# Kernel tuning notes

Hardware: AMD Instinct MI355X
Metric: run time of the kernel (lower is better)

## Reference

```python
import jax, jax.numpy as jnp
import numpy as np

V, B, H, NH = 3, 8192, 2048, 16
HD = H // NH
EPS = 1e-5


def setup_inputs() -> dict:
    key = jax.random.key(0)
    ks = jax.random.split(key, 20)
    s = 0.02
    d = {
        "views": jax.random.normal(ks[0], (V, B, H), jnp.float32),
        # per-view query/key/value projections (torch Linear: y = x @ W.T + b)
        "Wq": jax.random.normal(ks[1], (V, H, H)) * s, "bq": jnp.zeros((V, H)),
        "Wk": jax.random.normal(ks[2], (V, H, H)) * s, "bk": jnp.zeros((V, H)),
        "Wv": jax.random.normal(ks[3], (V, H, H)) * s, "bv": jnp.zeros((V, H)),
        # per-view MultiheadAttention internal in_proj (split into q/k/v) and out_proj
        "Wiq": jax.random.normal(ks[4], (V, H, H)) * s, "biq": jnp.zeros((V, H)),
        "Wik": jax.random.normal(ks[5], (V, H, H)) * s, "bik": jnp.zeros((V, H)),
        "Wiv": jax.random.normal(ks[6], (V, H, H)) * s, "biv": jnp.zeros((V, H)),
        "Wo": jax.random.normal(ks[7], (V, H, H)) * s, "bo": jnp.zeros((V, H)),
        # fusion output linear over concatenated views
        "Wout": jax.random.normal(ks[8], (H, V * H)) * s, "bout": jnp.zeros((H,)),
        # LayerNorm
        "gamma": jnp.ones((H,)), "beta": jnp.zeros((H,)),
    }
    return d


def reference(views, Wq, bq, Wk, bk, Wv, bv, Wiq, biq, Wik, bik, Wiv, biv,
              Wo, bo, Wout, bout, gamma, beta):
    # views: [V, B, H]
    # per-view q/k/v projections applied to each view's own embedding
    q = jnp.einsum('vbh,vgh->vbg', views, Wq) + bq[:, None]      # [V,B,H]
    k_all = jnp.einsum('vbh,vgh->vbg', views, Wk) + bk[:, None]  # [V,B,H]
    v_all = jnp.einsum('vbh,vgh->vbg', views, Wv) + bv[:, None]  # [V,B,H]

    # for query view i, keys/values come from all other views (static gather)
    others = jnp.asarray(np.array([[j for j in range(V) if j != i] for i in range(V)]))
    K = k_all[others]   # [V, V-1, B, H]
    Vv = v_all[others]  # [V, V-1, B, H]

    # MultiheadAttention internal in-projections (per query-view i)
    q2 = jnp.einsum('vbh,vgh->vbg', q, Wiq) + biq[:, None]                # [V,B,H]
    k2 = jnp.einsum('vjbh,vgh->vjbg', K, Wik) + bik[:, None, None]        # [V,V-1,B,H]
    v2 = jnp.einsum('vjbh,vgh->vjbg', Vv, Wiv) + biv[:, None, None]       # [V,V-1,B,H]

    qh = q2.reshape(V, B, NH, HD)           # q_len = 1 (squeezed)
    kh = k2.reshape(V, V - 1, B, NH, HD)
    vh = v2.reshape(V, V - 1, B, NH, HD)

    scores = jnp.einsum('vbnd,vjbnd->vbnj', qh, kh) / jnp.sqrt(jnp.float32(HD))
    attn = jax.nn.softmax(scores, axis=-1)  # over the V-1 key views
    ctx = jnp.einsum('vbnj,vjbnd->vbnd', attn, vh).reshape(V, B, H)
    att_out = jnp.einsum('vbh,vgh->vbg', ctx, Wo) + bo[:, None]           # [V,B,H]

    # concat attended outputs per-sample: [B, V*H]
    fused = att_out.transpose(1, 0, 2).reshape(B, V * H)
    projected = fused @ Wout.T + bout

    # residual with first view + LayerNorm (dropout inactive / eval)
    x = views[0] + projected
    mu = jnp.mean(x, axis=-1, keepdims=True)
    var = jnp.mean(jnp.square(x - mu), axis=-1, keepdims=True)
    out = (x - mu) * jax.lax.rsqrt(var + EPS) * gamma + beta
    return out
```

## Files before the change

kernel.cpp:

```cpp
#include <hip/hip_runtime.h>
#include <hip/hip_bf16.h>

typedef __attribute__((ext_vector_type(8))) __bf16 bf16x8;
typedef __attribute__((ext_vector_type(4))) float f32x4;
typedef __hip_bfloat16 bf16_t;

#define BB 8192L
#define HH 2048L
#define BH (8192L*2048L)
#define WUNIT (2048L*2048L)
#define WT (3L*2048L*2048L)
#define LDS_TOTAL 131072

struct SlabMap { int a[6]; int w[6]; };
struct Ptrs4 { const float* in[4]; bf16_t* out[4]; };
struct FoldJob { const float* W2; const float* b1; const float* badd; float* out; int ld; };
struct FoldPack { FoldJob j[16]; };

__device__ __forceinline__ void gload_lds16(const void* g, void* l) {
    __builtin_amdgcn_global_load_lds((__attribute__((address_space(1))) void*)g,
                                     (__attribute__((address_space(3))) void*)l, 16, 0, 0);
}

template<bool OUT_F32, bool FUSEK>
__global__ __launch_bounds__(512, 1)
void gemm256(const bf16_t* __restrict__ A, int lda, long aslab, SlabMap map, int mshift,
             const bf16_t* __restrict__ Bw, int ldb,
             const float* __restrict__ bias,
             void* __restrict__ Cout, int ldc, long cslab, int K)
{
    extern __shared__ char lds[];
    const int tid  = threadIdx.x;
    const int lane = tid & 63;
    const int w    = tid >> 6;
    const int wm   = w >> 2, wn = w & 3;

    const int nwg = (int)gridDim.x;
    const int wid = (int)blockIdx.x;
    const int swz = (wid & 7) * (nwg >> 3) + (wid >> 3);
    const int bx  = swz & 7;
    const int by  = swz >> 3;

    const int  sl    = by >> mshift;
    const long rowA0 = (long)(by & ((1 << mshift) - 1)) * 256;
    const long rowB0 = (long)bx * 256;
    const bf16_t* Ab = FUSEK ? A : (A + (long)map.a[sl] * aslab);
    const bf16_t* Wb = Bw + (long)map.w[sl] * WUNIT;
    const float*  be = bias ? (bias + (long)map.w[sl] * HH) : nullptr;

    const int srow    = tid >> 3;
    const int schunk8 = ((tid & 7) ^ (srow & 7)) * 8;
    const int wuni    = w * 1024;
    const int NK = K >> 6;

    auto stageA = [&](int s) {
        char* dst = lds + (s & 1) * 65536;
        const int k0 = s << 6;
        const bf16_t* Aeff; int ka;
        if constexpr (FUSEK) { Aeff = A + (long)(k0 >> 11) * aslab; ka = k0 & 2047; }
        else                 { Aeff = Ab; ka = k0; }
        #pragma unroll
        for (int i = 0; i < 4; ++i)
            gload_lds16(Aeff + (rowA0 + i*64 + srow) * (long)lda + (ka + schunk8), dst + i*8192 + wuni);
    };
    auto stageB = [&](int s, int q) {
        char* dst = lds + (s & 1) * 65536 + 32768 + q*16384;
        const int k0 = s << 6;
        #pragma unroll
        for (int j = 0; j < 2; ++j)
            gload_lds16(Wb + (rowB0 + q*128 + j*64 + srow) * (long)ldb + (k0 + schunk8), dst + j*8192 + wuni);
    };

    f32x4 acc[8][4];
    const f32x4 zero = {0.f, 0.f, 0.f, 0.f};
    #pragma unroll
    for (int i = 0; i < 8; ++i)
        #pragma unroll
        for (int j = 0; j < 4; ++j) acc[i][j] = zero;

    stageB(0,0); stageB(0,1);
    stageA(0);
    stageB(1,0); stageB(1,1);
    asm volatile("s_waitcnt vmcnt(4)" ::: "memory");
    asm volatile("s_barrier" ::: "memory");

    const int arow16 = wm*128 + (lane & 15);
    const int brow16 = wn*64  + (lane & 15);
    const int kb     = (lane >> 4) * 16;

    #define LDSA(row, kh) (*(const bf16x8*)(bufA + (row)*128 + (((kh)*64 + kb) ^ (((row) & 7) << 4))))
    #define LDSB(row, kh) (*(const bf16x8*)(bufB + (row)*128 + (((kh)*64 + kb) ^ (((row) & 7) << 4))))

    for (int s = 0; s < NK; ++s) {
        char* bufA = lds + (s & 1) * 65536;
        char* bufB = bufA + 32768;
        bf16x8 a[4][2], b0[2][2], b1[2][2];

        if (s + 1 < NK) stageA(s + 1);
        #pragma unroll
        for (int cf = 0; cf < 2; ++cf) {
            const int r = brow16 + cf*16;
            #pragma unroll
            for (int kh = 0; kh < 2; ++kh) b0[cf][kh] = LDSB(r, kh);
        }
        #pragma unroll
        for (int rf = 0; rf < 4; ++rf) {
            const int r = arow16 + rf*16;
            #pragma unroll
            for (int kh = 0; kh < 2; ++kh) a[rf][kh] = LDSA(r, kh);
        }
        asm volatile("s_barrier" ::: "memory");
        __builtin_amdgcn_sched_barrier(0);
        __builtin_amdgcn_s_setprio(1);
        #pragma unroll
        for (int kh = 0; kh < 2; ++kh)
            #pragma unroll
            for (int rf = 0; rf < 4; ++rf)
                #pragma unroll
                for (int cf = 0; cf < 2; ++cf)
                    acc[rf][cf] = __builtin_amdgcn_mfma_f32_16x16x32_bf16(a[rf][kh], b0[cf][kh], acc[rf][cf], 0, 0, 0);
        __builtin_amdgcn_s_setprio(0);

        #pragma unroll
        for (int cf = 0; cf < 2; ++cf) {
            const int r = brow16 + 32 + cf*16;
            #pragma unroll
            for (int kh = 0; kh < 2; ++kh) b1[cf][kh] = LDSB(r, kh);
        }
        asm volatile("s_barrier" ::: "memory");
        __builtin_amdgcn_sched_barrier(0);
        __builtin_amdgcn_s_setprio(1);
        #pragma unroll
        for (int kh = 0; kh < 2; ++kh)
            #pragma unroll
            for (int rf = 0; rf < 4; ++rf)
                #pragma unroll
                for (int cf = 0; cf < 2; ++cf)
                    acc[rf][2+cf] = __builtin_amdgcn_mfma_f32_16x16x32_bf16(a[rf][kh], b1[cf][kh], acc[rf][2+cf], 0, 0, 0);
        __builtin_amdgcn_s_setprio(0);

        if (s + 2 < NK) stageB(s + 2, 0);
        #pragma unroll
        for (int rf = 0; rf < 4; ++rf) {
            const int r = arow16 + 64 + rf*16;
            #pragma unroll
            for (int kh = 0; kh < 2; ++kh) a[rf][kh] = LDSA(r, kh);
        }
        asm volatile("s_barrier" ::: "memory");
        __builtin_amdgcn_sched_barrier(0);
        __builtin_amdgcn_s_setprio(1);
        #pragma unroll
        for (int kh = 0; kh < 2; ++kh)
            #pragma unroll
            for (int rf = 0; rf < 4; ++rf)
                #pragma unroll
                for (int cf = 0; cf < 2; ++cf)
                    acc[4+rf][cf] = __builtin_amdgcn_mfma_f32_16x16x32_bf16(a[rf][kh], b0[cf][kh], acc[4+rf][cf], 0, 0, 0);
        __builtin_amdgcn_s_setprio(0);

        if (s + 2 < NK) stageB(s + 2, 1);
        if (s + 1 < NK) {
            if (s + 2 < NK) asm volatile("s_waitcnt vmcnt(4)" ::: "memory");
            else            asm volatile("s_waitcnt vmcnt(0)" ::: "memory");
            asm volatile("s_barrier" ::: "memory");
            __builtin_amdgcn_sched_barrier(0);
        }
        __builtin_amdgcn_s_setprio(1);
        #pragma unroll
        for (int kh = 0; kh < 2; ++kh)
            #pragma unroll
            for (int rf = 0; rf < 4; ++rf)
                #pragma unroll
                for (int cf = 0; cf < 2; ++cf)
                    acc[4+rf][2+cf] = __builtin_amdgcn_mfma_f32_16x16x32_bf16(a[rf][kh], b1[cf][kh], acc[4+rf][2+cf], 0, 0, 0);
        __builtin_amdgcn_s_setprio(0);
    }
    #undef LDSA
    #undef LDSB

    const long crow0 = rowA0 + wm*128 + ((lane >> 4) * 4);
    const int  ccol0 = (int)rowB0 + wn*64 + (lane & 15);
    const long cbase = (long)sl * cslab;
    #pragma unroll
    for (int rf = 0; rf < 8; ++rf) {
        #pragma unroll
        for (int cf = 0; cf < 4; ++cf) {
            const int col = ccol0 + cf*16;
            const float bv = be ? be[col] : 0.f;
            #pragma unroll
            for (int r = 0; r < 4; ++r) {
                const long row = crow0 + rf*16 + r;
                const float val = acc[rf][cf][r] + bv;
                if constexpr (OUT_F32) ((float*)Cout)[cbase + row*(long)ldc + col] = val;
                else ((bf16_t*)Cout)[cbase + row*(long)ldc + col] = __float2bfloat16(val);
            }
        }
    }
}

__global__ __launch_bounds__(256)
void f2b_kernel(const float* __restrict__ in, bf16_t* __restrict__ out, long n)
{
    long i = ((long)blockIdx.x * 256 + threadIdx.x) * 4;
    const long stride = (long)gridDim.x * 256 * 4;
    for (; i < n; i += stride) {
        const float4 v = *(const float4*)(in + i);
        __hip_bfloat162 lo, hi;
        lo.x = __float2bfloat16(v.x); lo.y = __float2bfloat16(v.y);
        hi.x = __float2bfloat16(v.z); hi.y = __float2bfloat16(v.w);
        *(__hip_bfloat162*)(out + i)     = lo;
        *(__hip_bfloat162*)(out + i + 2) = hi;
    }
}

__global__ __launch_bounds__(256)
void f2b4_kernel(Ptrs4 p)
{
    const long total = 4 * WT;
    long i = ((long)blockIdx.x * 256 + threadIdx.x) * 4;
    const long stride = (long)gridDim.x * 256 * 4;
    for (; i < total; i += stride) {
        const int  t   = (int)(i / WT);
        const long off = i - (long)t * WT;
        const float4 v = *(const float4*)(p.in[t] + off);
        __hip_bfloat162 lo, hi;
        lo.x = __float2bfloat16(v.x); lo.y = __float2bfloat16(v.y);
        hi.x = __float2bfloat16(v.z); hi.y = __float2bfloat16(v.w);
        *(__hip_bfloat162*)(p.out[t] + off)     = lo;
        *(__hip_bfloat162*)(p.out[t] + off + 2) = hi;
    }
}

__global__ __launch_bounds__(256)
void f2bT4_kernel(Ptrs4 p)
{
    __shared__ float sm[64][65];
    const int gmat = blockIdx.x >> 10;
    const int t    = gmat / 3, m = gmat % 3;
    const int tile = blockIdx.x & 1023;
    const int tr   = tile >> 5, tc = tile & 31;
    const int lr = threadIdx.x >> 4;
    const int lc = (threadIdx.x & 15) * 4;
    const float* src = p.in[t] + (long)m*WUNIT + ((long)tr*64)*2048 + tc*64;
    #pragma unroll
    for (int it = 0; it < 4; ++it) {
        const int r = lr + it*16;
        const float4 v = *(const float4*)(src + (long)r*2048 + lc);
        sm[r][lc] = v.x; sm[r][lc+1] = v.y; sm[r][lc+2] = v.z; sm[r][lc+3] = v.w;
    }
    __syncthreads();
    bf16_t* dst = p.out[t] + (long)m*WUNIT + ((long)tc*64)*2048 + tr*64;
    #pragma unroll
    for (int it = 0; it < 4; ++it) {
        const int r = lr + it*16;
        __hip_bfloat162 p0, p1;
        p0.x = __float2bfloat16(sm[lc+0][r]); p0.y = __float2bfloat16(sm[lc+1][r]);
        p1.x = __float2bfloat16(sm[lc+2][r]); p1.y = __float2bfloat16(sm[lc+3][r]);
        *(__hip_bfloat162*)(dst + (long)r*2048 + lc)     = p0;
        *(__hip_bfloat162*)(dst + (long)r*2048 + lc + 2) = p1;
    }
}

__global__ __launch_bounds__(256)
void biasfold_all(FoldPack p)
{
    const FoldJob jb = p.j[blockIdx.x >> 11];
    const int g2 = blockIdx.x & 2047;
    const int t  = threadIdx.x;
    float s = 0.f;
    for (int k = t; k < jb.ld; k += 256) s += jb.W2[(long)g2*jb.ld + k] * jb.b1[k];
    #pragma unroll
    for (int off = 32; off > 0; off >>= 1) s += __shfl_xor(s, off);
    __shared__ float rs[4];
    if ((t & 63) == 0) rs[t >> 6] = s;
    __syncthreads();
    if (t == 0) jb.out[g2] = rs[0] + rs[1] + rs[2] + rs[3] + jb.badd[g2];
}

__global__ __launch_bounds__(256)
void attn_kernel(const bf16_t* __restrict__ q2, const bf16_t* __restrict__ k2,
                 const bf16_t* __restrict__ v2, bf16_t* __restrict__ ctx, int bshift)
{
    const long gw = (long)blockIdx.x * 4 + (threadIdx.x >> 6);
    const int lane = threadIdx.x & 63;
    const int  v_  = (int)(gw >> (bshift + 4));
    const long rem = gw & ((1L << (bshift + 4)) - 1);
    const long b   = rem >> 4;
    const int  n   = (int)(rem & 15);
    const long base = ((((long)v_ << bshift) + b)) * HH + (long)n * 128 + lane * 2;

    const __hip_bfloat162 qv = *(const __hip_bfloat162*)(q2 + base);
    const float q0 = __bfloat162float(qv.x), q1 = __bfloat162float(qv.y);
    float s[2], va[2], vb[2];
    #pragma unroll
    for (int j = 0; j < 2; ++j) {
        const long kb = ((((long)(v_*2 + j) << bshift) + b)) * HH + (long)n * 128 + lane * 2;
        const __hip_bfloat162 kv = *(const __hip_bfloat162*)(k2 + kb);
        float p = q0 * __bfloat162float(kv.x) + q1 * __bfloat162float(kv.y);
        #pragma unroll
        for (int off = 32; off > 0; off >>= 1) p += __shfl_xor(p, off);
        s[j] = p;
        const __hip_bfloat162 vv = *(const __hip_bfloat162*)(v2 + kb);
        va[j] = __bfloat162float(vv.x); vb[j] = __bfloat162float(vv.y);
    }
    const float scale = 0.08838834764831845f;
    const float s0 = s[0] * scale, s1 = s[1] * scale;
    const float m  = fmaxf(s0, s1);
    const float e0 = expf(s0 - m), e1 = expf(s1 - m);
    const float inv = 1.0f / (e0 + e1);
    const float a0 = e0 * inv, a1 = e1 * inv;
    __hip_bfloat162 o;
    o.x = __float2bfloat16(a0 * va[0] + a1 * va[1]);
    o.y = __float2bfloat16(a0 * vb[0] + a1 * vb[1]);
    *(__hip_bfloat162*)(ctx + base) = o;
}

__global__ __launch_bounds__(256)
void ln_kernel(const float* __restrict__ proj, const float* __restrict__ v0,
               const float* __restrict__ gamma, const float* __restrict__ beta,
               float* __restrict__ out)
{
    const long b = blockIdx.x;
    const int t = threadIdx.x;
    const float* pr = proj + b * HH;
    const float* vw = v0 + b * HH;
    float x[8]; float s = 0.f, s2 = 0.f;
    #pragma unroll
    for (int k = 0; k < 8; ++k) {
        const int idx = t + k * 256;
        x[k] = vw[idx] + pr[idx];
        s += x[k]; s2 += x[k] * x[k];
    }
    #pragma unroll
    for (int off = 32; off > 0; off >>= 1) { s += __shfl_xor(s, off); s2 += __shfl_xor(s2, off); }
    __shared__ float rs[4], rs2[4];
    if ((t & 63) == 0) { rs[t >> 6] = s; rs2[t >> 6] = s2; }
    __syncthreads();
    s  = rs[0] + rs[1] + rs[2] + rs[3];
    s2 = rs2[0] + rs2[1] + rs2[2] + rs2[3];
    const float mu  = s * (1.0f / 2048.0f);
    const float var = s2 * (1.0f / 2048.0f) - mu * mu;
    const float rstd = rsqrtf(var + 1e-5f);
    #pragma unroll
    for (int k = 0; k < 8; ++k) {
        const int idx = t + k * 256;
        out[b * HH + idx] = (x[k] - mu) * rstd * gamma[idx] + beta[idx];
    }
}

extern "C" void kernel_launch(void* const* d_in, const int* in_sizes, int n_in,
                              void* d_out, int out_size, void* d_ws, size_t ws_size,
                              hipStream_t stream)
{
    const float* views = (const float*)d_in[0];
    const float* Wq   = (const float*)d_in[1];  const float* bq   = (const float*)d_in[2];
    const float* Wk   = (const float*)d_in[3];  const float* bk   = (const float*)d_in[4];
    const float* Wv   = (const float*)d_in[5];  const float* bv   = (const float*)d_in[6];
    const float* Wiq  = (const float*)d_in[7];  const float* biq  = (const float*)d_in[8];
    const float* Wik  = (const float*)d_in[9];  const float* bik  = (const float*)d_in[10];
    const float* Wiv  = (const float*)d_in[11]; const float* biv  = (const float*)d_in[12];
    const float* Wo   = (const float*)d_in[13]; const float* bo   = (const float*)d_in[14];
    const float* Wout = (const float*)d_in[15]; const float* bout = (const float*)d_in[16];
    const float* gamma= (const float*)d_in[17]; const float* beta = (const float*)d_in[18];

    static bool attr_set = false;
    if (!attr_set) {
        hipFuncSetAttribute((const void*)gemm256<false,false>,
                            hipFuncAttributeMaxDynamicSharedMemorySize, LDS_TOTAL);
        hipFuncSetAttribute((const void*)gemm256<true,true>,
                            hipFuncAttributeMaxDynamicSharedMemorySize, LDS_TOTAL);
        attr_set = true;
    }

    char* ws = (char*)d_ws;
    bf16_t* WQ2  = (bf16_t*)ws;
    bf16_t* WK2  = WQ2 + 3*WUNIT;
    bf16_t* WV2  = WK2 + 6*WUNIT;
    bf16_t* WFIN = WV2 + 6*WUNIT;
    float*  BQ2  = (float*)(WFIN + 3*WUNIT);
    float*  BK2  = BQ2 + 3*HH;
    float*  BV2  = BK2 + 6*HH;
    float*  BFIN = BV2 + 6*HH;
    const long FIXED = 18L*WUNIT*2 + 16L*HH*4;

    char* R = ws + FIXED;
    bf16_t* WIQ   = (bf16_t*)R;
    bf16_t* WIK   = WIQ  + 3*WUNIT;
    bf16_t* WIV   = WIK  + 3*WUNIT;
    bf16_t* WOUTB = WIV  + 3*WUNIT;
    bf16_t* WQT   = WOUTB+ 3*WUNIT;
    bf16_t* WKT   = WQT  + 3*WUNIT;
    bf16_t* WVT   = WKT  + 3*WUNIT;
    bf16_t* WOT   = WVT  + 3*WUNIT;

    const long scratch = 24L*WUNIT*2;
    long Bc = 8192;
    while (Bc > 256) {
        long need = Bc * 73728L; if (need < scratch) need = scratch;
        if (FIXED + need <= (long)ws_size) break;
        Bc >>= 1;
    }
    const int mshift = __builtin_ctzl((unsigned long)Bc) - 8;
    const int bshift = __builtin_ctzl((unsigned long)Bc);
    const long S1 = Bc * HH;

    bf16_t* VBF = (bf16_t*)R;
    bf16_t* Q2B = VBF + 3*S1;
    bf16_t* K2  = Q2B + 3*S1;
    bf16_t* V2  = K2  + 6*S1;
    float*  PROJ= (float*)K2;

    const SlabMap mp3  = {{0,1,2,0,0,0},{0,1,2,0,0,0}};
    const SlabMap mp6k = {{1,2,0,2,0,1},{0,1,2,3,4,5}};
    const SlabMap mpfk = {{0,0,1,1,2,2},{1,2,0,2,0,1}};
    const SlabMap mp1  = {{0,0,0,0,0,0},{0,0,0,0,0,0}};
    const int oth[3][2] = {{1,2},{0,2},{0,1}};

    {
        Ptrs4 c1 = {{Wiq, Wik, Wiv, Wout}, {WIQ, WIK, WIV, WOUTB}};
        f2b4_kernel<<<8192, 256, 0, stream>>>(c1);
        Ptrs4 c2 = {{Wq, Wk, Wv, Wo}, {WQT, WKT, WVT, WOT}};
        f2bT4_kernel<<<12288, 256, 0, stream>>>(c2);
    }
    gemm256<false,false><<<192, 512, LDS_TOTAL, stream>>>(WIQ, 2048, WUNIT, mp3,  3, WQT, 2048, nullptr, (void*)WQ2, 2048, WUNIT, 2048);
    gemm256<false,false><<<384, 512, LDS_TOTAL, stream>>>(WIK, 2048, WUNIT, mpfk, 3, WKT, 2048, nullptr, (void*)WK2, 2048, WUNIT, 2048);
    gemm256<false,false><<<384, 512, LDS_TOTAL, stream>>>(WIV, 2048, WUNIT, mpfk, 3, WVT, 2048, nullptr, (void*)WV2, 2048, WUNIT, 2048);
    gemm256<false,false><<<192, 512, LDS_TOTAL, stream>>>(WOUTB, 6144, 2048, mp3, 3, WOT, 2048, nullptr, (void*)WFIN, 6144, 2048, 2048);

    {
        FoldPack fp;
        for (int v = 0; v < 3; ++v)
            fp.j[v] = { Wiq + (long)v*WUNIT, bq + v*HH, biq + v*HH, BQ2 + v*HH, 2048 };
        for (int v = 0; v < 3; ++v)
            for (int j = 0; j < 2; ++j) {
                const int p = v*2 + j, o = oth[v][j];
                fp.j[3 + p] = { Wik + (long)v*WUNIT, bk + o*HH, bik + v*HH, BK2 + p*HH, 2048 };
                fp.j[9 + p] = { Wiv + (long)v*WUNIT, bv + o*HH, biv + v*HH, BV2 + p*HH, 2048 };
            }
        fp.j[15] = { Wout, bo, bout, BFIN, 6144 };
        biasfold_all<<<32768, 256, 0, stream>>>(fp);
    }

    const int nwg3 = 8 * 3 * (int)(Bc >> 8);
    const int nwg6 = 8 * 6 * (int)(Bc >> 8);
    const int nwg1 = 8 * 1 * (int)(Bc >> 8);
    const int vgrid = (int)((S1 / 1024 > 8192) ? 8192 : S1 / 1024);

    for (long b0 = 0; b0 < BB; b0 += Bc) {
        if (Bc == 8192) {
            f2b_kernel<<<8192, 256, 0, stream>>>(views, VBF, 3*BH);
        } else {
            for (int v = 0; v < 3; ++v)
                f2b_kernel<<<vgrid, 256, 0, stream>>>(views + v*BH + b0*HH, VBF + v*S1, S1);
        }
        gemm256<false,false><<<nwg3, 512, LDS_TOTAL, stream>>>(VBF, 2048, S1, mp3,  mshift, WQ2, 2048, BQ2, (void*)Q2B, 2048, S1, 2048);
        gemm256<false,false><<<nwg6, 512, LDS_TOTAL, stream>>>(VBF, 2048, S1, mp6k, mshift, WK2, 2048, BK2, (void*)K2,  2048, S1, 2048);
        gemm256<false,false><<<nwg6, 512, LDS_TOTAL, stream>>>(VBF, 2048, S1, mp6k, mshift, WV2, 2048, BV2, (void*)V2,  2048, S1, 2048);
        attn_kernel<<<(int)(12*Bc), 256, 0, stream>>>(Q2B, K2, V2, VBF, bshift);
        gemm256<true,true><<<nwg1, 512, LDS_TOTAL, stream>>>(VBF, 2048, S1, mp1, mshift, WFIN, 6144, BFIN, (void*)PROJ, 2048, 0, 6144);
        ln_kernel<<<(int)Bc, 256, 0, stream>>>(PROJ, views + b0*HH, gamma, beta, ((float*)d_out) + b0*HH);
    }
}
```

Measured before the change: 1.699 ms.

## Triple-buffer A tiles in GEMM and merge weight-fold GEMMs into one launch

Result: faster. 1.647 ms (-3.1%).

```diff
diff --git a/kernel.cpp b/kernel.cpp
--- a/kernel.cpp
+++ b/kernel.cpp
@@ -10,16 +10,179 @@
 #define BH (8192L*2048L)
 #define WUNIT (2048L*2048L)
 #define WT (3L*2048L*2048L)
-#define LDS_TOTAL 131072
+#define LDS_TOTAL 163840
 
 struct SlabMap { int a[6]; int w[6]; };
 struct Ptrs4 { const float* in[4]; bf16_t* out[4]; };
 struct FoldJob { const float* W2; const float* b1; const float* badd; float* out; int ld; };
 struct FoldPack { FoldJob j[16]; };
+struct GJob { const bf16_t* A; const bf16_t* Bw; bf16_t* C; int lda; int ldc; };
+struct GJobs { GJob j[18]; };
 
 __device__ __forceinline__ void gload_lds16(const void* g, void* l) {
     __builtin_amdgcn_global_load_lds((__attribute__((address_space(1))) void*)g,
                                      (__attribute__((address_space(3))) void*)l, 16, 0, 0);
+}
+
+template<bool OUT_F32, bool FUSEK>
+__device__ __forceinline__ void gemm_core(
+    const bf16_t* __restrict__ A, int lda, long aslab,
+    const bf16_t* __restrict__ Wb, int ldb,
+    const float* __restrict__ be,
+    void* __restrict__ Cout, int ldc,
+    long rowA0, long rowB0, int K, char* lds)
+{
+    const int tid  = threadIdx.x;
+    const int lane = tid & 63;
+    const int w    = tid >> 6;
+    const int wm   = w >> 2, wn = w & 3;
+
+    const int srow    = tid >> 3;
+    const int schunk8 = ((tid & 7) ^ (srow & 7)) * 8;
+    const int wuni    = w * 1024;
+    const int NK = K >> 6;
+
+    auto stageA = [&](int s) {
+        char* dst = lds + (s % 3) * 32768;
+        const int k0 = s << 6;
+        const bf16_t* Aeff; int ka;
+        if constexpr (FUSEK) { Aeff = A + (long)(k0 >> 11) * aslab; ka = k0 & 2047; }
+        else                 { Aeff = A; ka = k0; }
+        #pragma unroll
+        for (int i = 0; i < 4; ++i)
+            gload_lds16(Aeff + (rowA0 + i*64 + srow) * (long)lda + (ka + schunk8), dst + i*8192 + wuni);
+    };
+    auto stageB = [&](int s, int q) {
+        char* dst = lds + 98304 + (s & 1) * 32768 + q*16384;
+        const int k0 = s << 6;
+        #pragma unroll
+        for (int j = 0; j < 2; ++j)
+            gload_lds16(Wb + (rowB0 + q*128 + j*64 + srow) * (long)ldb + (k0 + schunk8), dst + j*8192 + wuni);
+    };
+
+    f32x4 acc[8][4];
+    const f32x4 zero = {0.f, 0.f, 0.f, 0.f};
+    #pragma unroll
+    for (int i = 0; i < 8; ++i)
+        #pragma unroll
+        for (int j = 0; j < 4; ++j) acc[i][j] = zero;
+
+    stageA(0); stageB(0,0); stageB(0,1);
+    stageA(1); stageB(1,0); stageB(1,1);
+    asm volatile("s_waitcnt vmcnt(8)" ::: "memory");
+    asm volatile("s_barrier" ::: "memory");
+
+    const int arow16 = wm*128 + (lane & 15);
+    const int brow16 = wn*64  + (lane & 15);
+    const int kb     = (lane >> 4) * 16;
+
+    #define LDSA(row, kh) (*(const bf16x8*)(bufA + (row)*128 + (((kh)*64 + kb) ^ (((row) & 7) << 4))))
+    #define LDSB(row, kh) (*(const bf16x8*)(bufB + (row)*128 + (((kh)*64 + kb) ^ (((row) & 7) << 4))))
+
+    for (int s = 0; s < NK; ++s) {
+        char* bufA = lds + (s % 3) * 32768;
+        char* bufB = lds + 98304 + (s & 1) * 32768;
+        bf16x8 a[4][2], b0[2][2], b1[2][2];
+
+        if (s + 2 < NK) stageA(s + 2);
+        #pragma unroll
+        for (int cf = 0; cf < 2; ++cf) {
+            const int r = brow16 + cf*16;
+            #pragma unroll
+            for (int kh = 0; kh < 2; ++kh) b0[cf][kh] = LDSB(r, kh);
+        }
+        #pragma unroll
+        for (int rf = 0; rf < 4; ++rf) {
+            const int r = arow16 + rf*16;
+            #pragma unroll
+            for (int kh = 0; kh < 2; ++kh) a[rf][kh] = LDSA(r, kh);
+        }
+        asm volatile("s_barrier" ::: "memory");
+        __builtin_amdgcn_sched_barrier(0);
+        __builtin_amdgcn_s_setprio(1);
+        #pragma unroll
+        for (int kh = 0; kh < 2; ++kh)
+            #pragma unroll
+            for (int rf = 0; rf < 4; ++rf)
+                #pragma unroll
+                for (int cf = 0; cf < 2; ++cf)
+                    acc[rf][cf] = __builtin_amdgcn_mfma_f32_16x16x32_bf16(a[rf][kh], b0[cf][kh], acc[rf][cf], 0, 0, 0);
+        __builtin_amdgcn_s_setprio(0);
+
+        #pragma unroll
+        for (int cf = 0; cf < 2; ++cf) {
+            const int r = brow16 + 32 + cf*16;
+            #pragma unroll
+            for (int kh = 0; kh < 2; ++kh) b1[cf][kh] = LDSB(r, kh);
+        }
+        asm volatile("s_barrier" ::: "memory");
+        __builtin_amdgcn_sched_barrier(0);
+        __builtin_amdgcn_s_setprio(1);
+        #pragma unroll
+        for (int kh = 0; kh < 2; ++kh)
+            #pragma unroll
+            for (int rf = 0; rf < 4; ++rf)
+                #pragma unroll
+                for (int cf = 0; cf < 2; ++cf)
+                    acc[rf][2+cf] = __builtin_amdgcn_mfma_f32_16x16x32_bf16(a[rf][kh], b1[cf][kh], acc[rf][2+cf], 0, 0, 0);
+        __builtin_amdgcn_s_setprio(0);
+
+        if (s + 2 < NK) stageB(s + 2, 0);
+        #pragma unroll
+        for (int rf = 0; rf < 4; ++rf) {
+            const int r = arow16 + 64 + rf*16;
+            #pragma unroll
+            for (int kh = 0; kh < 2; ++kh) a[rf][kh] = LDSA(r, kh);
+        }
+        asm volatile("s_barrier" ::: "memory");
+        __builtin_amdgcn_sched_barrier(0);
+        __builtin_amdgcn_s_setprio(1);
+        #pragma unroll
+        for (int kh = 0; kh < 2; ++kh)
+            #pragma unroll
+            for (int rf = 0; rf < 4; ++rf)
+                #pragma unroll
+                for (int cf = 0; cf < 2; ++cf)
+                    acc[4+rf][cf] = __builtin_amdgcn_mfma_f32_16x16x32_bf16(a[rf][kh], b0[cf][kh], acc[4+rf][cf], 0, 0, 0);
+        __builtin_amdgcn_s_setprio(0);
+
+        if (s + 2 < NK) stageB(s + 2, 1);
+        if (s + 1 < NK) {
+            if (s + 2 < NK) asm volatile("s_waitcnt vmcnt(8)" ::: "memory");
+            else            asm volatile("s_waitcnt vmcnt(0)" ::: "memory");
+            asm volatile("s_barrier" ::: "memory");
+            __builtin_amdgcn_sched_barrier(0);
+        }
+        __builtin_amdgcn_s_setprio(1);
+        #pragma unroll
+        for (int kh = 0; kh < 2; ++kh)
+            #pragma unroll
+            for (int rf = 0; rf < 4; ++rf)
+                #pragma unroll
+                for (int cf = 0; cf < 2; ++cf)
+                    acc[4+rf][2+cf] = __builtin_amdgcn_mfma_f32_16x16x32_bf16(a[rf][kh], b1[cf][kh], acc[4+rf][2+cf], 0, 0, 0);
+        __builtin_amdgcn_s_setprio(0);
+    }
+    #undef LDSA
+    #undef LDSB
+
+    const long crow0 = rowA0 + wm*128 + ((lane >> 4) * 4);
+    const int  ccol0 = (int)rowB0 + wn*64 + (lane & 15);
+    #pragma unroll
+    for (int rf = 0; rf < 8; ++rf) {
+        #pragma unroll
+        for (int cf = 0; cf < 4; ++cf) {
+            const int col = ccol0 + cf*16;
+            const float bv = be ? be[col] : 0.f;
+            #pragma unroll
+            for (int r = 0; r < 4; ++r) {
+                const long row = crow0 + rf*16 + r;
+                const float val = acc[rf][cf][r] + bv;
+                if constexpr (OUT_F32) ((float*)Cout)[row*(long)ldc + col] = val;
+                else ((bf16_t*)Cout)[row*(long)ldc + col] = __float2bfloat16(val);
+            }
+        }
+    }
 }
 
 template<bool OUT_F32, bool FUSEK>
@@ -30,11 +193,6 @@
              void* __restrict__ Cout, int ldc, long cslab, int K)
 {
     extern __shared__ char lds[];
-    const int tid  = threadIdx.x;
-    const int lane = tid & 63;
-    const int w    = tid >> 6;
-    const int wm   = w >> 2, wn = w & 3;
-
     const int nwg = (int)gridDim.x;
     const int wid = (int)blockIdx.x;
     const int swz = (wid & 7) * (nwg >> 3) + (wid >> 3);
@@ -47,155 +205,24 @@
     const bf16_t* Ab = FUSEK ? A : (A + (long)map.a[sl] * aslab);
     const bf16_t* Wb = Bw + (long)map.w[sl] * WUNIT;
     const float*  be = bias ? (bias + (long)map.w[sl] * HH) : nullptr;
-
-    const int srow    = tid >> 3;
-    const int schunk8 = ((tid & 7) ^ (srow & 7)) * 8;
-    const int wuni    = w * 1024;
-    const int NK = K >> 6;
-
-    auto stageA = [&](int s) {
-        char* dst = lds + (s & 1) * 65536;
-        const int k0 = s << 6;
-        const bf16_t* Aeff; int ka;
-        if constexpr (FUSEK) { Aeff = A + (long)(k0 >> 11) * aslab; ka = k0 & 2047; }
-        else                 { Aeff = Ab; ka = k0; }
-        #pragma unroll
-        for (int i = 0; i < 4; ++i)
-            gload_lds16(Aeff + (rowA0 + i*64 + srow) * (long)lda + (ka + schunk8), dst + i*8192 + wuni);
-    };
-    auto stageB = [&](int s, int q) {
-        char* dst = lds + (s & 1) * 65536 + 32768 + q*16384;
-        const int k0 = s << 6;
-        #pragma unroll
-        for (int j = 0; j < 2; ++j)
-            gload_lds16(Wb + (rowB0 + q*128 + j*64 + srow) * (long)ldb + (k0 + schunk8), dst + j*8192 + wuni);
-    };
-
-    f32x4 acc[8][4];
-    const f32x4 zero = {0.f, 0.f, 0.f, 0.f};
-    #pragma unroll
-    for (int i = 0; i < 8; ++i)
-        #pragma unroll
-        for (int j = 0; j < 4; ++j) acc[i][j] = zero;
-
-    stageB(0,0); stageB(0,1);
-    stageA(0);
-    stageB(1,0); stageB(1,1);
-    asm volatile("s_waitcnt vmcnt(4)" ::: "memory");
-    asm volatile("s_barrier" ::: "memory");
-
-    const int arow16 = wm*128 + (lane & 15);
-    const int brow16 = wn*64  + (lane & 15);
-    const int kb     = (lane >> 4) * 16;
-
-    #define LDSA(row, kh) (*(const bf16x8*)(bufA + (row)*128 + (((kh)*64 + kb) ^ (((row) & 7) << 4))))
-    #define LDSB(row, kh) (*(const bf16x8*)(bufB + (row)*128 + (((kh)*64 + kb) ^ (((row) & 7) << 4))))
-
-    for (int s = 0; s < NK; ++s) {
-        char* bufA = lds + (s & 1) * 65536;
-        char* bufB = bufA + 32768;
-        bf16x8 a[4][2], b0[2][2], b1[2][2];
-
-        if (s + 1 < NK) stageA(s + 1);
-        #pragma unroll
-        for (int cf = 0; cf < 2; ++cf) {
-            const int r = brow16 + cf*16;
-            #pragma unroll
-            for (int kh = 0; kh < 2; ++kh) b0[cf][kh] = LDSB(r, kh);
-        }
-        #pragma unroll
-        for (int rf = 0; rf < 4; ++rf) {
-            const int r = arow16 + rf*16;
-            #pragma unroll
-            for (int kh = 0; kh < 2; ++kh) a[rf][kh] = LDSA(r, kh);
-        }
-        asm volatile("s_barrier" ::: "memory");
-        __builtin_amdgcn_sched_barrier(0);
-        __builtin_amdgcn_s_setprio(1);
-        #pragma unroll
-        for (int kh = 0; kh < 2; ++kh)
-            #pragma unroll
-            for (int rf = 0; rf < 4; ++rf)
-                #pragma unroll
-                for (int cf = 0; cf < 2; ++cf)
-                    acc[rf][cf] = __builtin_amdgcn_mfma_f32_16x16x32_bf16(a[rf][kh], b0[cf][kh], acc[rf][cf], 0, 0, 0);
-        __builtin_amdgcn_s_setprio(0);
-
-        #pragma unroll
-        for (int cf = 0; cf < 2; ++cf) {
-            const int r = brow16 + 32 + cf*16;
-            #pragma unroll
-            for (int kh = 0; kh < 2; ++kh) b1[cf][kh] = LDSB(r, kh);
-        }
-        asm volatile("s_barrier" ::: "memory");
-        __builtin_amdgcn_sched_barrier(0);
-        __builtin_amdgcn_s_setprio(1);
-        #pragma unroll
-        for (int kh = 0; kh < 2; ++kh)
-            #pragma unroll
-            for (int rf = 0; rf < 4; ++rf)
-                #pragma unroll
-                for (int cf = 0; cf < 2; ++cf)
-                    acc[rf][2+cf] = __builtin_amdgcn_mfma_f32_16x16x32_bf16(a[rf][kh], b1[cf][kh], acc[rf][2+cf], 0, 0, 0);
-        __builtin_amdgcn_s_setprio(0);
-
-        if (s + 2 < NK) stageB(s + 2, 0);
-        #pragma unroll
-        for (int rf = 0; rf < 4; ++rf) {
-            const int r = arow16 + 64 + rf*16;
-            #pragma unroll
-            for (int kh = 0; kh < 2; ++kh) a[rf][kh] = LDSA(r, kh);
-        }
-        asm volatile("s_barrier" ::: "memory");
-        __builtin_amdgcn_sched_barrier(0);
-        __builtin_amdgcn_s_setprio(1);
-        #pragma unroll
-        for (int kh = 0; kh < 2; ++kh)
-            #pragma unroll
-            for (int rf = 0; rf < 4; ++rf)
-                #pragma unroll
-                for (int cf = 0; cf < 2; ++cf)
-                    acc[4+rf][cf] = __builtin_amdgcn_mfma_f32_16x16x32_bf16(a[rf][kh], b0[cf][kh], acc[4+rf][cf], 0, 0, 0);
-        __builtin_amdgcn_s_setprio(0);
-
-        if (s + 2 < NK) stageB(s + 2, 1);
-        if (s + 1 < NK) {
-            if (s + 2 < NK) asm volatile("s_waitcnt vmcnt(4)" ::: "memory");
-            else            asm volatile("s_waitcnt vmcnt(0)" ::: "memory");
-            asm volatile("s_barrier" ::: "memory");
-            __builtin_amdgcn_sched_barrier(0);
-        }
-        __builtin_amdgcn_s_setprio(1);
-        #pragma unroll
-        for (int kh = 0; kh < 2; ++kh)
-            #pragma unroll
-            for (int rf = 0; rf < 4; ++rf)
-                #pragma unroll
-                for (int cf = 0; cf < 2; ++cf)
-                    acc[4+rf][2+cf] = __builtin_amdgcn_mfma_f32_16x16x32_bf16(a[rf][kh], b1[cf][kh], acc[4+rf][2+cf], 0, 0, 0);
-        __builtin_amdgcn_s_setprio(0);
-    }
-    #undef LDSA
-    #undef LDSB
-
-    const long crow0 = rowA0 + wm*128 + ((lane >> 4) * 4);
-    const int  ccol0 = (int)rowB0 + wn*64 + (lane & 15);
     const long cbase = (long)sl * cslab;
-    #pragma unroll
-    for (int rf = 0; rf < 8; ++rf) {
-        #pragma unroll
-        for (int cf = 0; cf < 4; ++cf) {
-            const int col = ccol0 + cf*16;
-            const float bv = be ? be[col] : 0.f;
-            #pragma unroll
-            for (int r = 0; r < 4; ++r) {
-                const long row = crow0 + rf*16 + r;
-                const float val = acc[rf][cf][r] + bv;
-                if constexpr (OUT_F32) ((float*)Cout)[cbase + row*(long)ldc + col] = val;
-                else ((bf16_t*)Cout)[cbase + row*(long)ldc + col] = __float2bfloat16(val);
-            }
-        }
-    }
+    void* Cj = OUT_F32 ? (void*)((float*)Cout + cbase) : (void*)((bf16_t*)Cout + cbase);
+    gemm_core<OUT_F32, FUSEK>(Ab, lda, aslab, Wb, ldb, be, Cj, ldc, rowA0, rowB0, K, lds);
+}
+
+__global__ __launch_bounds__(512, 1)
+void gemm_fold(GJobs js)
+{
+    extern __shared__ char lds[];
+    const int nwg = (int)gridDim.x;
+    const int wid = (int)blockIdx.x;
+    const int swz = (wid & 7) * (nwg >> 3) + (wid >> 3);
+    const GJob jb = js.j[swz >> 6];
+    const int inner = swz & 63;
+    const long rowA0 = (long)(inner >> 3) * 256;
+    const long rowB0 = (long)(inner & 7) * 256;
+    gemm_core<false, false>(jb.A, jb.lda, 0L, jb.Bw, 2048, nullptr,
+                            (void*)jb.C, jb.ldc, rowA0, rowB0, 2048, lds);
 }
 
 __global__ __launch_bounds__(256)
@@ -369,6 +396,8 @@
                             hipFuncAttributeMaxDynamicSharedMemorySize, LDS_TOTAL);
         hipFuncSetAttribute((const void*)gemm256<true,true>,
                             hipFuncAttributeMaxDynamicSharedMemorySize, LDS_TOTAL);
+        hipFuncSetAttribute((const void*)gemm_fold,
+                            hipFuncAttributeMaxDynamicSharedMemorySize, LDS_TOTAL);
         attr_set = true;
     }
 
@@ -412,7 +441,6 @@
 
     const SlabMap mp3  = {{0,1,2,0,0,0},{0,1,2,0,0,0}};
     const SlabMap mp6k = {{1,2,0,2,0,1},{0,1,2,3,4,5}};
-    const SlabMap mpfk = {{0,0,1,1,2,2},{1,2,0,2,0,1}};
     const SlabMap mp1  = {{0,0,0,0,0,0},{0,0,0,0,0,0}};
     const int oth[3][2] = {{1,2},{0,2},{0,1}};
 
@@ -422,11 +450,20 @@
         Ptrs4 c2 = {{Wq, Wk, Wv, Wo}, {WQT, WKT, WVT, WOT}};
         f2bT4_kernel<<<12288, 256, 0, stream>>>(c2);
     }
-    gemm256<false,false><<<192, 512, LDS_TOTAL, stream>>>(WIQ, 2048, WUNIT, mp3,  3, WQT, 2048, nullptr, (void*)WQ2, 2048, WUNIT, 2048);
-    gemm256<false,false><<<384, 512, LDS_TOTAL, stream>>>(WIK, 2048, WUNIT, mpfk, 3, WKT, 2048, nullptr, (void*)WK2, 2048, WUNIT, 2048);
-    gemm256<false,false><<<384, 512, LDS_TOTAL, stream>>>(WIV, 2048, WUNIT, mpfk, 3, WVT, 2048, nullptr, (void*)WV2, 2048, WUNIT, 2048);
-    gemm256<false,false><<<192, 512, LDS_TOTAL, stream>>>(WOUTB, 6144, 2048, mp3, 3, WOT, 2048, nullptr, (void*)WFIN, 6144, 2048, 2048);
-
+    {
+        GJobs js;
+        for (int v = 0; v < 3; ++v)
+            js.j[v] = { WIQ + (long)v*WUNIT, WQT + (long)v*WUNIT, WQ2 + (long)v*WUNIT, 2048, 2048 };
+        for (int v = 0; v < 3; ++v)
+            for (int j = 0; j < 2; ++j) {
+                const int p = v*2 + j, o = oth[v][j];
+                js.j[3 + p] = { WIK + (long)v*WUNIT, WKT + (long)o*WUNIT, WK2 + (long)p*WUNIT, 2048, 2048 };
+                js.j[9 + p] = { WIV + (long)v*WUNIT, WVT + (long)o*WUNIT, WV2 + (long)p*WUNIT, 2048, 2048 };
+            }
+        for (int v = 0; v < 3; ++v)
+            js.j[15 + v] = { WOUTB + (long)v*2048, WOT + (long)v*WUNIT, WFIN + (long)v*2048, 6144, 6144 };
+        gemm_fold<<<1152, 512, LDS_TOTAL, stream>>>(js);
+    }
     {
         FoldPack fp;
         for (int v = 0; v < 3; ++v)
```
